# Optimization experiments

Hardware: AMD Instinct MI355X
Metric: run time of the kernel (lower is better)

## Reference

```python
import jax, jax.numpy as jnp
import numpy as np

K = 1024          # num_embeddings
D = 256           # embedding_dim
COMMIT = 0.25
DECAY = 0.99
EPS = 1e-05


def setup_inputs() -> dict:
    key = jax.random.key(0)
    k1, k2 = jax.random.split(key)
    inputs = jax.random.normal(k1, (16, 4096, D), dtype=jnp.float32)
    weight = jax.random.normal(k2, (K, D), dtype=jnp.float32) * 0.1
    ema_cluster_size = jnp.zeros((K,), dtype=jnp.float32)
    ema_embedding_avg = weight  # initialized as a clone of the weights
    return {
        "inputs": inputs,
        "weight": weight,
        "ema_cluster_size": ema_cluster_size,
        "ema_embedding_avg": ema_embedding_avg,
    }


def reference(inputs, weight, ema_cluster_size, ema_embedding_avg):
    B = inputs.shape[0]
    flat = inputs.reshape(-1, D)                      # [N, D]
    dist = (
        jnp.sum(flat * flat, axis=1, keepdims=True)
        + jnp.sum(weight * weight, axis=1)
        - 2.0 * (flat @ weight.T)
    )                                                 # [N, K]
    idx = jnp.argmin(dist, axis=1)                    # [N] int
    # one-hot @ weight == gather
    quantized = weight[idx].reshape(inputs.shape)

    # --- EMA codebook update (training-mode side effects, returned as outputs) ---
    counts = jax.ops.segment_sum(jnp.ones_like(idx, dtype=jnp.float32), idx, num_segments=K)
    emb_sum = jax.ops.segment_sum(flat, idx, num_segments=K)  # one_hot.T @ flat
    new_cluster_size = DECAY * ema_cluster_size + (1.0 - DECAY) * counts
    new_embedding_avg = DECAY * ema_embedding_avg + (1.0 - DECAY) * emb_sum
    n = jnp.sum(new_cluster_size)
    cs = (new_cluster_size + EPS) / (n + K * EPS) * n
    new_weight = new_embedding_avg / cs[:, None]

    # --- losses + straight-through estimator ---
    e_latent_loss = jnp.mean((jax.lax.stop_gradient(quantized) - inputs) ** 2)
    q_latent_loss = jnp.mean((quantized - jax.lax.stop_gradient(inputs)) ** 2)
    vq_loss = q_latent_loss + COMMIT * e_latent_loss
    quantized_st = inputs + jax.lax.stop_gradient(quantized - inputs)

    return (
        quantized_st,
        vq_loss,
        idx.reshape(B, -1),
        new_weight,
        new_cluster_size,
        new_embedding_avg,
    )
```

## Files before the change

### kernel.cpp

```cpp
#include <hip/hip_runtime.h>

#define KC 1024
#define DD 256
#define NROWS 65536
#define BM 128
#define NT 256
#define RESCUE_EPS 0.02f
#define RB 8

typedef _Float16 f16x8 __attribute__((ext_vector_type(8)));
typedef __fp16 fp16x2 __attribute__((ext_vector_type(2)));
typedef float f32x4 __attribute__((ext_vector_type(4)));
typedef const __attribute__((address_space(1))) unsigned int* gptr_t;
typedef __attribute__((address_space(3))) unsigned int* lptr_t;

__global__ void wprep(const float* __restrict__ W, _Float16* __restrict__ wh,
                      float* __restrict__ se, float4* __restrict__ WT4,
                      float* __restrict__ counts, double* __restrict__ loss,
                      int* __restrict__ flagcnt) {
    int k = blockIdx.x, lane = threadIdx.x;
    float4 v = reinterpret_cast<const float4*>(W + (size_t)k * DD)[lane];
    union { fp16x2 h2[2]; uint2 u; } cv;
    cv.h2[0] = __builtin_amdgcn_cvt_pkrtz(v.x, v.y);
    cv.h2[1] = __builtin_amdgcn_cvt_pkrtz(v.z, v.w);
    *reinterpret_cast<uint2*>(wh + (size_t)k * DD + lane * 4) = cv.u;
    WT4[(size_t)lane * KC + k] = v;
    double s = (double)v.x * v.x + (double)v.y * v.y + (double)v.z * v.z + (double)v.w * v.w;
    for (int m = 32; m >= 1; m >>= 1) s += __shfl_xor(s, m, 64);
    if (lane == 0) {
        se[k] = (float)s;
        counts[k] = 0.0f;
        if (k == 0) { loss[0] = 0.0; flagcnt[0] = 0; }
    }
}

__global__ __launch_bounds__(NT, 2) void vq_mfma(
    const float* __restrict__ X,
    const _Float16* __restrict__ wh,
    const float* __restrict__ se,
    float* __restrict__ out_q, float* __restrict__ out_idx,
    int* __restrict__ idx_int, float* __restrict__ sx_out,
    int* __restrict__ flags, int* __restrict__ count,
    float* __restrict__ counts, double* __restrict__ loss_acc)
{
    __shared__ __align__(16) _Float16 wt[2][64 * 256];
    __shared__ float sxs[BM];
    __shared__ float ses[KC];
    __shared__ int argidx[BM];
    __shared__ double lred[4];

    const int tid = threadIdx.x;
    const int row0 = blockIdx.x * BM;
    const int w = tid >> 6, lane = tid & 63;
    const int m = lane & 15, g = lane >> 4;

    for (int i = tid; i < KC; i += NT) ses[i] = se[i];

    f16x8 ahr[2][8];
#pragma unroll
    for (int rt = 0; rt < 2; ++rt) {
        const float* xr = X + (size_t)(row0 + w * 32 + rt * 16 + m) * DD;
        float p0 = 0.f, p1 = 0.f, p2 = 0.f, p3 = 0.f;
#pragma unroll
        for (int ks = 0; ks < 8; ++ks) {
            float4 a = *reinterpret_cast<const float4*>(xr + ks * 32 + g * 8);
            float4 b = *reinterpret_cast<const float4*>(xr + ks * 32 + g * 8 + 4);
            union { fp16x2 h2[4]; f16x8 h8; } cv;
            cv.h2[0] = __builtin_amdgcn_cvt_pkrtz(a.x, a.y);
            cv.h2[1] = __builtin_amdgcn_cvt_pkrtz(a.z, a.w);
            cv.h2[2] = __builtin_amdgcn_cvt_pkrtz(b.x, b.y);
            cv.h2[3] = __builtin_amdgcn_cvt_pkrtz(b.z, b.w);
            ahr[rt][ks] = cv.h8;
            p0 = fmaf(a.x, a.x, fmaf(b.x, b.x, p0));
            p1 = fmaf(a.y, a.y, fmaf(b.y, b.y, p1));
            p2 = fmaf(a.z, a.z, fmaf(b.z, b.z, p2));
            p3 = fmaf(a.w, a.w, fmaf(b.w, b.w, p3));
        }
        float ss = (p0 + p1) + (p2 + p3);
        ss += __shfl_xor(ss, 16, 64);
        ss += __shfl_xor(ss, 32, 64);
        if (g == 0) sxs[w * 32 + rt * 16 + m] = ss;
    }

    unsigned srcoff[8], ldsoff[8];
#pragma unroll
    for (int p = 0; p < 8; ++p) {
        int gi = p * NT + tid;
        int code = gi >> 5, j = gi & 31;
        int kq = j ^ (code & 31);
        srcoff[p] = (unsigned)(code * DD + kq * 8);
        ldsoff[p] = gi * 8;
    }
    auto stage = [&](int ct, int buf) {
        const _Float16* b = wh + (size_t)ct * 64 * DD;
#pragma unroll
        for (int p = 0; p < 8; ++p)
            __builtin_amdgcn_global_load_lds((gptr_t)(const void*)(b + srcoff[p]),
                                             (lptr_t)(void*)&wt[buf][ldsoff[p]], 16, 0, 0);
    };

    stage(0, 0);
    __syncthreads();

    float b1[2][4], b2[2][4];
    int i1[2][4];
#pragma unroll
    for (int rt = 0; rt < 2; ++rt)
#pragma unroll
        for (int j = 0; j < 4; ++j) { b1[rt][j] = 3.4e38f; b2[rt][j] = 3.4e38f; i1[rt][j] = 0; }

    float sxr[2][4];
#pragma unroll
    for (int rt = 0; rt < 2; ++rt)
#pragma unroll
        for (int j = 0; j < 4; ++j) sxr[rt][j] = sxs[w * 32 + rt * 16 + g * 4 + j];

    for (int ct = 0; ct < 16; ++ct) {
        const int buf = ct & 1;
        if (ct < 15) stage(ct + 1, buf ^ 1);

        const _Float16* wtb = wt[buf];
        f32x4 acc0[4], acc1[4];
#pragma unroll
        for (int cs = 0; cs < 4; ++cs) {
            acc0[cs] = (f32x4){0.f, 0.f, 0.f, 0.f};
            acc1[cs] = (f32x4){0.f, 0.f, 0.f, 0.f};
        }

#pragma unroll
        for (int ks = 0; ks < 8; ++ks) {
            const int kq = ks * 4 + g;
#pragma unroll
            for (int cs = 0; cs < 4; ++cs) {
                const int code = cs * 16 + m;
                const int L = code * 32 + (kq ^ (code & 31));
                f16x8 bh = *reinterpret_cast<const f16x8*>(wtb + L * 8);
                acc0[cs] = __builtin_amdgcn_mfma_f32_16x16x32_f16(ahr[0][ks], bh, acc0[cs], 0, 0, 0);
                acc1[cs] = __builtin_amdgcn_mfma_f32_16x16x32_f16(ahr[1][ks], bh, acc1[cs], 0, 0, 0);
            }
        }
#pragma unroll
        for (int cs = 0; cs < 4; ++cs) {
            const int code = ct * 64 + cs * 16 + m;
            const float sec = ses[code];
#pragma unroll
            for (int rt = 0; rt < 2; ++rt) {
                f32x4 A = rt ? acc1[cs] : acc0[cs];
#pragma unroll
                for (int j = 0; j < 4; ++j) {
                    float s = fmaf(-2.0f, A[j], sxr[rt][j] + sec);
                    if (s < b1[rt][j]) { b2[rt][j] = b1[rt][j]; b1[rt][j] = s; i1[rt][j] = code; }
                    else if (s < b2[rt][j]) { b2[rt][j] = s; }
                }
            }
        }
        __syncthreads();
    }

#pragma unroll
    for (int rt = 0; rt < 2; ++rt)
#pragma unroll
        for (int j = 0; j < 4; ++j) {
            float v1 = b1[rt][j], v2 = b2[rt][j];
            int ix = i1[rt][j];
            for (int mm = 1; mm < 16; mm <<= 1) {
                float ov1 = __shfl_xor(v1, mm, 64);
                int oi = __shfl_xor(ix, mm, 64);
                float ov2 = __shfl_xor(v2, mm, 64);
                float nv2 = fminf(fminf(v2, ov2), fmaxf(v1, ov1));
                if (ov1 < v1 || (ov1 == v1 && oi < ix)) { v1 = ov1; ix = oi; }
                v2 = nv2;
            }
            if (m == 0) {
                int rl = w * 32 + rt * 16 + g * 4 + j;
                argidx[rl] = ix;
                if (v2 - v1 < RESCUE_EPS) {
                    int p = atomicAdd(count, 1);
                    flags[p] = row0 + rl;
                }
            }
        }
    __syncthreads();

    if (tid < BM) {
        int row = row0 + tid;
        int k = argidx[tid];
        idx_int[row] = k;
        out_idx[row] = (float)k;
        sx_out[row] = sxs[tid];
        atomicAdd(&counts[k], 1.0f);
    }

    {
        float lacc = 0.0f;
#pragma unroll
        for (int rt = 0; rt < 2; ++rt) {
            const int rl = w * 32 + rt * 16 + m;
            const int row = row0 + rl;
            const int k = argidx[rl];
            const _Float16* qh = wh + (size_t)k * DD;
            float* orow = out_q + (size_t)row * DD;
#pragma unroll
            for (int ks = 0; ks < 8; ++ks) {
                const int col = ks * 32 + g * 8;
                union { uint4 u; _Float16 h[8]; } qv, xv;
                qv.u = *reinterpret_cast<const uint4*>(qh + col);
                xv.u = *reinterpret_cast<uint4*>(&ahr[rt][ks]);
                float o8[8];
#pragma unroll
                for (int q = 0; q < 8; ++q) {
                    float qf = (float)qv.h[q];
                    float df = qf - (float)xv.h[q];
                    o8[q] = qf;
                    lacc = fmaf(df, df, lacc);
                }
                *reinterpret_cast<float4*>(orow + col)     = *reinterpret_cast<float4*>(&o8[0]);
                *reinterpret_cast<float4*>(orow + col + 4) = *reinterpret_cast<float4*>(&o8[4]);
            }
        }
        for (int mm = 32; mm >= 1; mm >>= 1) lacc += __shfl_xor(lacc, mm, 64);
        if (lane == 0) lred[w] = (double)lacc;
    }
    __syncthreads();
    if (tid == 0) {
        double t = lred[0] + lred[1] + lred[2] + lred[3];
        atomicAdd(loss_acc, t);
    }
}

__global__ __launch_bounds__(256) void rescue(
    const float* __restrict__ X, const float4* __restrict__ WT4,
    const float* __restrict__ Wf,
    const float* __restrict__ se, const float* __restrict__ sx,
    const int* __restrict__ flags, const int* __restrict__ count,
    int* __restrict__ idx_int, float* __restrict__ out_idx,
    float* __restrict__ out_q, float* __restrict__ counts,
    double* __restrict__ loss_acc)
{
    __shared__ __align__(16) float xs[RB][DD];
    __shared__ float rv[RB][256];
    __shared__ int ri[RB][256];
    __shared__ float sxr_s[RB];
    __shared__ int rows_s[RB];
    __shared__ int kn_s[RB], ko_s[RB];
    __shared__ double dred[4];
    const int t = threadIdx.x;
    const int n = count[0];

    for (int base = blockIdx.x * RB; base < n; base += gridDim.x * RB) {
        const int nb = min(RB, n - base);
        for (int idx = t; idx < nb * 64; idx += 256) {
            int r = idx >> 6, c4 = idx & 63;
            float4 v = reinterpret_cast<const float4*>(X + (size_t)flags[base + r] * DD)[c4];
            *reinterpret_cast<float4*>(&xs[r][c4 * 4]) = v;
        }
        if (t < nb) { rows_s[t] = flags[base + t]; sxr_s[t] = sx[flags[base + t]]; }
        __syncthreads();

        float acc[4][RB];
#pragma unroll
        for (int cc = 0; cc < 4; ++cc)
#pragma unroll
            for (int r = 0; r < RB; ++r) acc[cc][r] = 0.0f;

        float4 wv[4], wn[4];
#pragma unroll
        for (int cc = 0; cc < 4; ++cc) wv[cc] = WT4[(size_t)0 * KC + cc * 256 + t];

        for (int d4 = 0; d4 < 64; ++d4) {
            const int dn = (d4 < 63) ? d4 + 1 : 63;
#pragma unroll
            for (int cc = 0; cc < 4; ++cc) wn[cc] = WT4[(size_t)dn * KC + cc * 256 + t];
#pragma unroll
            for (int r = 0; r < RB; ++r) {
                float4 xv = *reinterpret_cast<const float4*>(&xs[r][d4 * 4]);
#pragma unroll
                for (int cc = 0; cc < 4; ++cc)
                    acc[cc][r] = fmaf(xv.w, wv[cc].w, fmaf(xv.z, wv[cc].z,
                                 fmaf(xv.y, wv[cc].y, fmaf(xv.x, wv[cc].x, acc[cc][r]))));
            }
#pragma unroll
            for (int cc = 0; cc < 4; ++cc) wv[cc] = wn[cc];
        }

        float best[RB];
        int bidx[RB];
#pragma unroll
        for (int r = 0; r < RB; ++r) { best[r] = 3.4e38f; bidx[r] = 0; }
#pragma unroll
        for (int cc = 0; cc < 4; ++cc) {
            const int c = cc * 256 + t;
            const float sec = se[c];
#pragma unroll
            for (int r = 0; r < RB; ++r) {
                float s = __fsub_rn(__fadd_rn(sxr_s[r], sec), __fmul_rn(2.0f, acc[cc][r]));
                if (s < best[r] || (s == best[r] && c < bidx[r])) { best[r] = s; bidx[r] = c; }
            }
        }
#pragma unroll
        for (int r = 0; r < RB; ++r) { rv[r][t] = best[r]; ri[r][t] = bidx[r]; }
        __syncthreads();

        for (int sft = 128; sft >= 1; sft >>= 1) {
            if (t < sft) {
#pragma unroll
                for (int r = 0; r < RB; ++r) {
                    float ov = rv[r][t + sft];
                    int oi = ri[r][t + sft];
                    if (ov < rv[r][t] || (ov == rv[r][t] && oi < ri[r][t])) {
                        rv[r][t] = ov; ri[r][t] = oi;
                    }
                }
            }
            __syncthreads();
        }
        if (t < nb) {
            int row = rows_s[t];
            int kn = ri[t][0], ko = idx_int[row];
            kn_s[t] = kn; ko_s[t] = ko;
            if (kn != ko) {
                idx_int[row] = kn;
                out_idx[row] = (float)kn;
                atomicAdd(&counts[ko], -1.0f);
                atomicAdd(&counts[kn], 1.0f);
            }
        }
        __syncthreads();

        for (int r = 0; r < nb; ++r) {
            const int ko = ko_s[r], kn = kn_s[r];
            if (kn != ko) {
                const int row = rows_s[r];
                float x = xs[r][t];
                float qo = Wf[(size_t)ko * DD + t];
                float qn = Wf[(size_t)kn * DD + t];
                float dfn = qn - x, dfo = qo - x;
                out_q[(size_t)row * DD + t] = x + dfn;
                double dl = (double)dfn * dfn - (double)dfo * dfo;
                for (int mm = 32; mm >= 1; mm >>= 1) dl += __shfl_xor(dl, mm, 64);
                if ((t & 63) == 0) dred[t >> 6] = dl;
                __syncthreads();
                if (t == 0) atomicAdd(loss_acc, dred[0] + dred[1] + dred[2] + dred[3]);
                __syncthreads();
            }
        }
        __syncthreads();
    }
}

__global__ void finprefix(const float* __restrict__ ema_cs, float* __restrict__ ncs_buf,
                          const double* __restrict__ loss_acc, float* __restrict__ out_loss,
                          float* __restrict__ n_out, int* __restrict__ off,
                          int* __restrict__ cur)
{
    __shared__ float red[1024];
    __shared__ int s[1024];
    int t = threadIdx.x;
    const float OM = (float)(1.0 - 0.99);
    float cnt = ncs_buf[t];
    s[t] = (int)cnt;
    float ncs = __fadd_rn(__fmul_rn(0.99f, ema_cs[t]), __fmul_rn(OM, cnt));
    ncs_buf[t] = ncs;
    red[t] = ncs;
    __syncthreads();
    for (int st = 512; st >= 1; st >>= 1) {
        if (t < st) red[t] += red[t + st];
        __syncthreads();
    }
    if (t == 0) {
        n_out[0] = red[0];
        float el = (float)(loss_acc[0] / 16777216.0);
        out_loss[0] = __fadd_rn(el, __fmul_rn(0.25f, el));
    }
    for (int d = 1; d < 1024; d <<= 1) {
        int v = (t >= d) ? s[t - d] : 0;
        __syncthreads();
        s[t] += v;
        __syncthreads();
    }
    off[t] = (t == 0) ? 0 : s[t - 1];
    cur[t] = 0;
    if (t == 0) off[1024] = NROWS;
}

__global__ __launch_bounds__(256) void scatter_rows(
    const int* __restrict__ idx_int, const int* __restrict__ off,
    int* __restrict__ cur, int* __restrict__ sorted) {
    int i = blockIdx.x * 256 + threadIdx.x;
    int k = idx_int[i];
    int p = atomicAdd(&cur[k], 1);
    sorted[off[k] + p] = i;
}

__global__ __launch_bounds__(256) void embfin2(
    const float* __restrict__ X, const int* __restrict__ off,
    const int* __restrict__ sorted, const float* __restrict__ ema_avg,
    const float* __restrict__ ncs, const float* __restrict__ n_ptr,
    float* __restrict__ out_avg, float* __restrict__ out_w)
{
    const int k = blockIdx.x, t = threadIdx.x;
    const int s0 = off[k], s1 = off[k + 1];
    float a0 = 0.f, a1 = 0.f, a2 = 0.f, a3 = 0.f;
    int i = s0;
    for (; i + 4 <= s1; i += 4) {
        int r0 = sorted[i], r1 = sorted[i + 1], r2 = sorted[i + 2], r3 = sorted[i + 3];
        a0 += X[(size_t)r0 * DD + t];
        a1 += X[(size_t)r1 * DD + t];
        a2 += X[(size_t)r2 * DD + t];
        a3 += X[(size_t)r3 * DD + t];
    }
    for (; i < s1; ++i) a0 += X[(size_t)sorted[i] * DD + t];
    float total = (a0 + a1) + (a2 + a3);

    const float OM = (float)(1.0 - 0.99);
    const float KEPS = (float)(1024.0 * 1e-5);
    size_t o = (size_t)k * DD + t;
    float avg = __fadd_rn(__fmul_rn(0.99f, ema_avg[o]), __fmul_rn(OM, total));
    float n = n_ptr[0];
    float cs = __fmul_rn(__fdiv_rn(__fadd_rn(ncs[k], 1e-5f), __fadd_rn(n, KEPS)), n);
    out_avg[o] = avg;
    out_w[o] = __fdiv_rn(avg, cs);
}

extern "C" void kernel_launch(void* const* d_in, const int* in_sizes, int n_in,
                              void* d_out, int out_size, void* d_ws, size_t ws_size,
                              hipStream_t stream) {
    const float* X = (const float*)d_in[0];
    const float* W = (const float*)d_in[1];
    const float* ema_cs = (const float*)d_in[2];
    const float* ema_avg = (const float*)d_in[3];

    float* out = (float*)d_out;
    float* out_q    = out;
    float* out_loss = out + 16777216;
    float* out_idx  = out + 16777217;
    float* out_w    = out + 16842753;
    float* out_ncs  = out + 17104897;
    float* out_avg  = out + 17105921;

    char* ws = (char*)d_ws;
    float* se      = (float*)(ws + 0);
    float* n_ptr   = (float*)(ws + 4096);
    double* loss   = (double*)(ws + 4112);
    int*   count   = (int*)(ws + 4128);
    _Float16* wh   = (_Float16*)(ws + 8192);
    float* sx      = (float*)(ws + 1056768);
    int*   idx_int = (int*)(ws + 1318912);
    int*   flags   = (int*)(ws + 1581056);
    float4* WT4    = (float4*)(ws + 2097152);
    int*   off     = (int*)(ws + 3145728);
    int*   cur     = (int*)(ws + 3153920);
    int*   sorted  = (int*)(ws + 3158016);

    wprep<<<KC, 64, 0, stream>>>(W, wh, se, WT4, out_ncs, loss, count);
    vq_mfma<<<NROWS / BM, NT, 0, stream>>>(X, wh, se, out_q, out_idx,
                                           idx_int, sx, flags, count,
                                           out_ncs, loss);
    rescue<<<512, 256, 0, stream>>>(X, WT4, W, se, sx, flags, count, idx_int, out_idx,
                                    out_q, out_ncs, loss);
    finprefix<<<1, 1024, 0, stream>>>(ema_cs, out_ncs, loss, out_loss, n_ptr, off, cur);
    scatter_rows<<<NROWS / 256, 256, 0, stream>>>(idx_int, off, cur, sorted);
    embfin2<<<KC, 256, 0, stream>>>(X, off, sorted, ema_avg, out_ncs, n_ptr,
                                    out_avg, out_w);
}
```

Measured before the change: 175.8 us.

## Give each wavefront private codebook tiles to drop block-wide barriers in the main loop

Each wavefront now stages its own 16-code slices of the fp16 codebook into a private double buffer, synchronising with explicit waitcnt instead of __syncthreads every tile. The loop runs 64 smaller tiles with one accumulator pair each, in place of 16 tiles with four. The aim is to remove the block-wide barrier stalls and let waves drift apart. The cost is that each wave loads the whole codebook itself, so global/L2 traffic into LDS is four times higher. There are also fewer independent MFMA chains per tile to hide latency.

Result: slower. 193.6 us (+10.1%).

```diff
diff --git a/kernel.cpp b/kernel.cpp
--- a/kernel.cpp
+++ b/kernel.cpp
@@ -43,7 +43,7 @@
     int* __restrict__ flags, int* __restrict__ count,
     float* __restrict__ counts, double* __restrict__ loss_acc)
 {
-    __shared__ __align__(16) _Float16 wt[2][64 * 256];
+    __shared__ __align__(16) _Float16 wt[4][2][16 * 256];
     __shared__ float sxs[BM];
     __shared__ float ses[KC];
     __shared__ int argidx[BM];
@@ -81,26 +81,30 @@
         ss += __shfl_xor(ss, 32, 64);
         if (g == 0) sxs[w * 32 + rt * 16 + m] = ss;
     }
+    __syncthreads();
+
+    float sxr[2][4];
+#pragma unroll
+    for (int rt = 0; rt < 2; ++rt)
+#pragma unroll
+        for (int j = 0; j < 4; ++j) sxr[rt][j] = sxs[w * 32 + rt * 16 + g * 4 + j];
 
     unsigned srcoff[8], ldsoff[8];
 #pragma unroll
     for (int p = 0; p < 8; ++p) {
-        int gi = p * NT + tid;
+        int gi = p * 64 + lane;
         int code = gi >> 5, j = gi & 31;
-        int kq = j ^ (code & 31);
+        int kq = j ^ code;
         srcoff[p] = (unsigned)(code * DD + kq * 8);
         ldsoff[p] = gi * 8;
     }
     auto stage = [&](int ct, int buf) {
-        const _Float16* b = wh + (size_t)ct * 64 * DD;
+        const _Float16* b = wh + (size_t)ct * 16 * DD;
 #pragma unroll
         for (int p = 0; p < 8; ++p)
             __builtin_amdgcn_global_load_lds((gptr_t)(const void*)(b + srcoff[p]),
-                                             (lptr_t)(void*)&wt[buf][ldsoff[p]], 16, 0, 0);
+                                             (lptr_t)(void*)&wt[w][buf][ldsoff[p]], 16, 0, 0);
     };
-
-    stage(0, 0);
-    __syncthreads();
 
     float b1[2][4], b2[2][4];
     int i1[2][4];
@@ -109,52 +113,41 @@
 #pragma unroll
         for (int j = 0; j < 4; ++j) { b1[rt][j] = 3.4e38f; b2[rt][j] = 3.4e38f; i1[rt][j] = 0; }
 
-    float sxr[2][4];
-#pragma unroll
-    for (int rt = 0; rt < 2; ++rt)
-#pragma unroll
-        for (int j = 0; j < 4; ++j) sxr[rt][j] = sxs[w * 32 + rt * 16 + g * 4 + j];
-
-    for (int ct = 0; ct < 16; ++ct) {
-        const int buf = ct & 1;
-        if (ct < 15) stage(ct + 1, buf ^ 1);
-
-        const _Float16* wtb = wt[buf];
-        f32x4 acc0[4], acc1[4];
-#pragma unroll
-        for (int cs = 0; cs < 4; ++cs) {
-            acc0[cs] = (f32x4){0.f, 0.f, 0.f, 0.f};
-            acc1[cs] = (f32x4){0.f, 0.f, 0.f, 0.f};
-        }
-
+    stage(0, 0);
+    int buf = 0;
+    for (int ct = 0; ct < 64; ++ct) {
+        if (ct < 63) {
+            asm volatile("s_waitcnt lgkmcnt(0)" ::: "memory");
+            stage(ct + 1, buf ^ 1);
+            asm volatile("s_waitcnt vmcnt(8)" ::: "memory");
+        } else {
+            asm volatile("s_waitcnt vmcnt(0)" ::: "memory");
+        }
+        __builtin_amdgcn_sched_barrier(0);
+
+        const _Float16* wtb = wt[w][buf];
+        f32x4 acc0 = {0.f, 0.f, 0.f, 0.f}, acc1 = {0.f, 0.f, 0.f, 0.f};
 #pragma unroll
         for (int ks = 0; ks < 8; ++ks) {
             const int kq = ks * 4 + g;
-#pragma unroll
-            for (int cs = 0; cs < 4; ++cs) {
-                const int code = cs * 16 + m;
-                const int L = code * 32 + (kq ^ (code & 31));
-                f16x8 bh = *reinterpret_cast<const f16x8*>(wtb + L * 8);
-                acc0[cs] = __builtin_amdgcn_mfma_f32_16x16x32_f16(ahr[0][ks], bh, acc0[cs], 0, 0, 0);
-                acc1[cs] = __builtin_amdgcn_mfma_f32_16x16x32_f16(ahr[1][ks], bh, acc1[cs], 0, 0, 0);
-            }
-        }
-#pragma unroll
-        for (int cs = 0; cs < 4; ++cs) {
-            const int code = ct * 64 + cs * 16 + m;
-            const float sec = ses[code];
-#pragma unroll
-            for (int rt = 0; rt < 2; ++rt) {
-                f32x4 A = rt ? acc1[cs] : acc0[cs];
-#pragma unroll
-                for (int j = 0; j < 4; ++j) {
-                    float s = fmaf(-2.0f, A[j], sxr[rt][j] + sec);
-                    if (s < b1[rt][j]) { b2[rt][j] = b1[rt][j]; b1[rt][j] = s; i1[rt][j] = code; }
-                    else if (s < b2[rt][j]) { b2[rt][j] = s; }
-                }
-            }
-        }
-        __syncthreads();
+            const int L = m * 32 + (kq ^ m);
+            f16x8 bh = *reinterpret_cast<const f16x8*>(wtb + L * 8);
+            acc0 = __builtin_amdgcn_mfma_f32_16x16x32_f16(ahr[0][ks], bh, acc0, 0, 0, 0);
+            acc1 = __builtin_amdgcn_mfma_f32_16x16x32_f16(ahr[1][ks], bh, acc1, 0, 0, 0);
+        }
+        const int code = ct * 16 + m;
+        const float sec = ses[code];
+#pragma unroll
+        for (int rt = 0; rt < 2; ++rt) {
+            f32x4 A = rt ? acc1 : acc0;
+#pragma unroll
+            for (int j = 0; j < 4; ++j) {
+                float s = fmaf(-2.0f, A[j], sxr[rt][j] + sec);
+                if (s < b1[rt][j]) { b2[rt][j] = b1[rt][j]; b1[rt][j] = s; i1[rt][j] = code; }
+                else if (s < b2[rt][j]) { b2[rt][j] = s; }
+            }
+        }
+        buf ^= 1;
     }
 
 #pragma unroll
```
